# Optimization experiments

Hardware: AMD Instinct MI355X
Metric: run time of the kernel (lower is better)

Reference implementation:

```python
import jax, jax.numpy as jnp
import numpy as np

N = 100000   # nodes
E = 1600000  # edges (avg degree 16)
D = 64       # channels (in = hidden = out)
L = 3        # layers


def setup_inputs() -> dict:
    key = jax.random.key(0)
    ks = jax.random.split(key, 8)
    s = 1.0 / np.sqrt(D)
    x = jax.random.normal(ks[0], (N, D), jnp.float32)
    edge_index = jax.random.randint(ks[1], (2, E), 0, N, dtype=jnp.int32)
    edge_type = jax.random.randint(ks[2], (E,), 0, 5, dtype=jnp.int32)
    Wq = jax.random.normal(ks[3], (L, D, D), jnp.float32) * s
    Wk = jax.random.normal(ks[4], (L, D, D), jnp.float32) * s
    Wv = jax.random.normal(ks[5], (L, D, D), jnp.float32) * s
    Ws = jax.random.normal(ks[6], (L, D, D), jnp.float32) * s
    bq = jnp.zeros((L, D), jnp.float32)
    bk = jnp.zeros((L, D), jnp.float32)
    bv = jnp.zeros((L, D), jnp.float32)
    bs = jnp.zeros((L, D), jnp.float32)
    return {"x": x, "edge_index": edge_index, "edge_type": edge_type,
            "Wq": Wq, "bq": bq, "Wk": Wk, "bk": bk,
            "Wv": Wv, "bv": bv, "Ws": Ws, "bs": bs}


def _transformer_conv(x, src, dst, Wq, bq, Wk, bk, Wv, bv, Ws, bs):
    # PyG TransformerConv, heads=1, concat=True, root_weight=True, beta=False
    q = x @ Wq + bq            # [N, D]
    k = x @ Wk + bk            # [N, D]
    v = x @ Wv + bv            # [N, D]
    scale = 1.0 / jnp.sqrt(jnp.asarray(D, x.dtype))
    # per-edge attention logits: <q_i, k_j> / sqrt(D)
    alpha = jnp.sum(q[dst] * k[src], axis=-1) * scale   # [E]
    # scatter-softmax over incoming edges of each target node
    m = jax.ops.segment_max(alpha, dst, num_segments=N)  # [N]
    e = jnp.exp(alpha - m[dst])                          # [E]
    denom = jax.ops.segment_sum(e, dst, num_segments=N)  # [N]
    a = e / (denom[dst] + 1e-16)                         # [E]
    # scatter-add aggregation of alpha * v_j
    agg = jax.ops.segment_sum(a[:, None] * v[src], dst, num_segments=N)  # [N, D]
    # root/skip connection (lin_skip with bias)
    return agg + x @ Ws + bs


def reference(x, edge_index, edge_type, Wq, bq, Wk, bk, Wv, bv, Ws, bs):
    src, dst = edge_index[0], edge_index[1]
    h = x
    for i in range(L):
        h = _transformer_conv(h, src, dst, Wq[i], bq[i], Wk[i], bk[i],
                              Wv[i], bv[i], Ws[i], bs[i])
        if i < L - 1:
            h = jax.nn.relu(h)
            # F.dropout(p=0.4) is identity in eval mode
    return h
```

## Files before the change

### kernel.cpp

```cpp
#include <hip/hip_runtime.h>

#define D 64
#define LAYERS 3
#define BSHIFT 8
#define NBMAX 512
#define CHUNK 4096

typedef unsigned short ushort_t;
typedef __bf16 bf16x8 __attribute__((ext_vector_type(8)));
typedef float f32x4 __attribute__((ext_vector_type(4)));

__device__ __forceinline__ ushort_t f2bf(float f) {
    unsigned b = __float_as_uint(f);
    b += 0x7FFFu + ((b >> 16) & 1u);
    return (ushort_t)(b >> 16);
}
__device__ __forceinline__ float bflo(unsigned u) { return __uint_as_float(u << 16); }
__device__ __forceinline__ float bfhi(unsigned u) { return __uint_as_float(u & 0xFFFF0000u); }

__global__ __launch_bounds__(256) void conv_kernel(
    const float* __restrict__ x, ushort_t* __restrict__ xb, int n,
    const float* __restrict__ Wq, const float* __restrict__ Wk,
    const float* __restrict__ Wv, const float* __restrict__ Ws,
    ushort_t* __restrict__ wtb)
{
    const int t = threadIdx.x;
    if (blockIdx.x < LAYERS * 4) {
        const int b = blockIdx.x;
        const int l = b >> 2, m = b & 3;
        const float* W = ((m == 0) ? Wq : (m == 1) ? Wk : (m == 2) ? Wv : Ws)
                         + (size_t)l * D * D;
        ushort_t* out = wtb + (size_t)b * D * D;
#pragma unroll
        for (int i = 0; i < 16; ++i) {
            const int e = i * 256 + t;
            const int nn = e >> 6, k = e & 63;
            out[nn * D + k] = f2bf(W[k * D + nn]);
        }
    } else {
        const int g = (blockIdx.x - LAYERS * 4) * 256 + t;
        const int i = g * 8;
        if (i >= n) return;
        const float4 x0 = *(const float4*)(x + i);
        const float4 x1 = *(const float4*)(x + i + 4);
        uint4 u;
        u.x = (unsigned)f2bf(x0.x) | ((unsigned)f2bf(x0.y) << 16);
        u.y = (unsigned)f2bf(x0.z) | ((unsigned)f2bf(x0.w) << 16);
        u.z = (unsigned)f2bf(x1.x) | ((unsigned)f2bf(x1.y) << 16);
        u.w = (unsigned)f2bf(x1.z) | ((unsigned)f2bf(x1.w) << 16);
        *(uint4*)(xb + i) = u;
    }
}

__global__ __launch_bounds__(256) void proj_kernel(
    const ushort_t* __restrict__ hb,
    const ushort_t* __restrict__ wtb_l,
    const float* __restrict__ bq, const float* __restrict__ bk,
    const float* __restrict__ bv, const float* __restrict__ bs,
    ushort_t* __restrict__ qb, ushort_t* __restrict__ kv,
    ushort_t* __restrict__ sk, int N)
{
    __shared__ ushort_t outq[32][72];
    __shared__ ushort_t outs[32][72];
    __shared__ ushort_t outkv[32][136];

    const int t = threadIdx.x;
    const int block_row = blockIdx.x * 32;
    const int l  = t & 63;
    const int w  = t >> 6;
    const int lr = l & 15;
    const int hi = l >> 4;
    const int lk = hi * 8;

    bf16x8 afr[2][2];
#pragma unroll
    for (int rt = 0; rt < 2; ++rt) {
        const int row = block_row + rt * 16 + lr;
        const size_t base = (size_t)min(row, N - 1) * D;
#pragma unroll
        for (int ks = 0; ks < 2; ++ks)
            afr[rt][ks] = *(const bf16x8*)(hb + base + ks * 32 + lk);
    }

    const ushort_t* wtw = wtb_l + (size_t)w * D * D;
    f32x4 acc[2][4];
#pragma unroll
    for (int rt = 0; rt < 2; ++rt)
#pragma unroll
        for (int ct = 0; ct < 4; ++ct)
            acc[rt][ct] = (f32x4){0.f, 0.f, 0.f, 0.f};

#pragma unroll
    for (int ct = 0; ct < 4; ++ct) {
        const bf16x8 b0 = *(const bf16x8*)(wtw + (ct * 16 + lr) * D + lk);
        const bf16x8 b1 = *(const bf16x8*)(wtw + (ct * 16 + lr) * D + 32 + lk);
        acc[0][ct] = __builtin_amdgcn_mfma_f32_16x16x32_bf16(afr[0][0], b0, acc[0][ct], 0, 0, 0);
        acc[0][ct] = __builtin_amdgcn_mfma_f32_16x16x32_bf16(afr[0][1], b1, acc[0][ct], 0, 0, 0);
        acc[1][ct] = __builtin_amdgcn_mfma_f32_16x16x32_bf16(afr[1][0], b0, acc[1][ct], 0, 0, 0);
        acc[1][ct] = __builtin_amdgcn_mfma_f32_16x16x32_bf16(afr[1][1], b1, acc[1][ct], 0, 0, 0);
    }

    const float* biasW = (w == 0) ? bq : (w == 1) ? bk : (w == 2) ? bv : bs;
    float bcol[4];
#pragma unroll
    for (int ct = 0; ct < 4; ++ct) bcol[ct] = biasW[ct * 16 + lr];

#pragma unroll
    for (int rt = 0; rt < 2; ++rt) {
#pragma unroll
        for (int ct = 0; ct < 4; ++ct) {
#pragma unroll
            for (int r = 0; r < 4; ++r) {
                const int row = rt * 16 + hi * 4 + r;
                const int col = ct * 16 + lr;
                const ushort_t vb = f2bf(acc[rt][ct][r] + bcol[ct]);
                if (w == 0)      outq[row][col] = vb;
                else if (w == 3) outs[row][col] = vb;
                else             outkv[row][(col >> 2) * 8 + ((w == 2) ? 4 : 0) + (col & 3)] = vb;
            }
        }
    }
    __syncthreads();

    const int row  = t >> 3;
    const int ch   = (t & 7) * 8;
    const int ckv  = (t & 7) * 16;
    const int grow = block_row + row;
    if (grow < N) {
        *(uint4*)(qb + (size_t)grow * 64 + ch)       = *(const uint4*)&outq[row][ch];
        *(uint4*)(sk + (size_t)grow * 64 + ch)       = *(const uint4*)&outs[row][ch];
        *(uint4*)(kv + (size_t)grow * 128 + ckv)     = *(const uint4*)&outkv[row][ckv];
        *(uint4*)(kv + (size_t)grow * 128 + ckv + 8) = *(const uint4*)&outkv[row][ckv + 8];
    }
}

__global__ __launch_bounds__(256) void b_hist_kernel(
    const int* __restrict__ dst, int* __restrict__ bcount, int E)
{
    __shared__ int h[NBMAX];
    const int t = threadIdx.x;
    h[t] = 0; h[t + 256] = 0;
    __syncthreads();
    const int base = blockIdx.x * CHUNK;
#pragma unroll
    for (int i = 0; i < 16; ++i) {
        const int e = base + i * 256 + t;
        if (e < E) atomicAdd(h + (dst[e] >> BSHIFT), 1);
    }
    __syncthreads();
    if (h[t])       atomicAdd(bcount + t, h[t]);
    if (h[t + 256]) atomicAdd(bcount + t + 256, h[t + 256]);
}

__global__ __launch_bounds__(512) void b_scan_kernel(
    const int* __restrict__ bcount, int* __restrict__ bbase,
    int* __restrict__ gcursor, int E)
{
    __shared__ int tmp[NBMAX];
    const int t = threadIdx.x;
    const int val = bcount[t];
    tmp[t] = val;
    __syncthreads();
    for (int off = 1; off < NBMAX; off <<= 1) {
        int x = (t >= off) ? tmp[t - off] : 0;
        __syncthreads();
        tmp[t] += x;
        __syncthreads();
    }
    const int excl = tmp[t] - val;
    bbase[t] = excl;
    gcursor[t] = excl;
    if (t == NBMAX - 1) bbase[NBMAX] = E;
}

__global__ __launch_bounds__(256) void b_scatter_kernel(
    const int* __restrict__ src, const int* __restrict__ dst,
    int* __restrict__ gcursor, unsigned* __restrict__ packed, int E)
{
    __shared__ int h[NBMAX];
    __shared__ int gb[NBMAX];
    const int t = threadIdx.x;
    h[t] = 0; h[t + 256] = 0;
    __syncthreads();

    const int base = blockIdx.x * CHUNK;
    int ls[16], ld[16], lr[16];
#pragma unroll
    for (int i = 0; i < 16; ++i) {
        const int e = base + i * 256 + t;
        if (e < E) {
            ls[i] = src[e];
            ld[i] = dst[e];
            lr[i] = atomicAdd(h + (ld[i] >> BSHIFT), 1);
        }
    }
    __syncthreads();
    for (int b = t; b < NBMAX; b += 256) {
        const int c = h[b];
        gb[b] = c ? atomicAdd(gcursor + b, c) : 0;
    }
    __syncthreads();
#pragma unroll
    for (int i = 0; i < 16; ++i) {
        const int e = base + i * 256 + t;
        if (e < E) {
            const int pos = gb[ld[i] >> BSHIFT] + lr[i];
            packed[pos] = ((unsigned)(ld[i] & 255) << 24) | (unsigned)ls[i];
        }
    }
}

__global__ __launch_bounds__(256) void b_final_kernel(
    const unsigned* __restrict__ packed, const int* __restrict__ bbase,
    int* __restrict__ esrc, int* __restrict__ offs, int* __restrict__ counts,
    int N)
{
    __shared__ int hist[256];
    __shared__ int scan[256];
    __shared__ int cursor[256];
    const int t = threadIdx.x;
    const int b = blockIdx.x;
    const int s = bbase[b];
    const int e = bbase[b + 1];

    hist[t] = 0;
    __syncthreads();
    for (int j = s + t; j < e; j += 256) {
        atomicAdd(hist + (packed[j] >> 24), 1);
    }
    __syncthreads();
    const int val = hist[t];
    scan[t] = val;
    __syncthreads();
    for (int off = 1; off < 256; off <<= 1) {
        int x = (t >= off) ? scan[t - off] : 0;
        __syncthreads();
        scan[t] += x;
        __syncthreads();
    }
    const int excl = scan[t] - val;
    const int node = b * 256 + t;
    if (node < N) {
        counts[node] = val;
        offs[node]   = s + excl;
    }
    cursor[t] = excl;
    __syncthreads();
    for (int j = s + t; j < e; j += 256) {
        const unsigned p = packed[j];
        const int r = atomicAdd(cursor + (p >> 24), 1);
        esrc[s + r] = (int)(p & 0xFFFFFFu);
    }
}

__global__ __launch_bounds__(256) void node_kernel(
    const ushort_t* __restrict__ qb, const uint4* __restrict__ kv,
    const int* __restrict__ esrc, const int* __restrict__ offs,
    const int* __restrict__ counts, const ushort_t* __restrict__ sk,
    ushort_t* __restrict__ hb_out, float* __restrict__ hf_out,
    int N, int mode)
{
    const int t = threadIdx.x;
    const int lane = t & 15;
    const int node = blockIdx.x * 16 + (t >> 4);
    if (node >= N) return;

    const int start = offs[node];
    const int end   = start + counts[node];

    const uint2 qu = *(const uint2*)(qb + (size_t)node * D + lane * 4);
    float4 qv;
    qv.x = bflo(qu.x); qv.y = bfhi(qu.x);
    qv.z = bflo(qu.y); qv.w = bfhi(qu.y);

    float m = -INFINITY, ssum = 0.0f;
    float4 acc = make_float4(0.0f, 0.0f, 0.0f, 0.0f);

    int j = start;
    for (; j + 2 <= end; j += 2) {
        const int s0 = esrc[j];
        const int s1 = esrc[j + 1];
        const uint4 u0 = kv[(size_t)s0 * 16 + lane];
        const uint4 u1 = kv[(size_t)s1 * 16 + lane];

        float p0 = bflo(u0.x) * qv.x + bfhi(u0.x) * qv.y
                 + bflo(u0.y) * qv.z + bfhi(u0.y) * qv.w;
        float p1 = bflo(u1.x) * qv.x + bfhi(u1.x) * qv.y
                 + bflo(u1.y) * qv.z + bfhi(u1.y) * qv.w;
        p0 += __shfl_xor(p0, 1);  p1 += __shfl_xor(p1, 1);
        p0 += __shfl_xor(p0, 2);  p1 += __shfl_xor(p1, 2);
        p0 += __shfl_xor(p0, 4);  p1 += __shfl_xor(p1, 4);
        p0 += __shfl_xor(p0, 8);  p1 += __shfl_xor(p1, 8);
        p0 *= 0.125f;  p1 *= 0.125f;

        const float mx = fmaxf(p0, p1);
        if (mx > m) {
            const float sc = __expf(m - mx);
            ssum *= sc;
            acc.x *= sc; acc.y *= sc; acc.z *= sc; acc.w *= sc;
            m = mx;
        }
        const float w0 = __expf(p0 - m);
        const float w1 = __expf(p1 - m);
        ssum += w0 + w1;
        acc.x = fmaf(w0, bflo(u0.z), fmaf(w1, bflo(u1.z), acc.x));
        acc.y = fmaf(w0, bfhi(u0.z), fmaf(w1, bfhi(u1.z), acc.y));
        acc.z = fmaf(w0, bflo(u0.w), fmaf(w1, bflo(u1.w), acc.z));
        acc.w = fmaf(w0, bfhi(u0.w), fmaf(w1, bfhi(u1.w), acc.w));
    }
    if (j < end) {
        const int s0 = esrc[j];
        const uint4 u0 = kv[(size_t)s0 * 16 + lane];
        float p0 = bflo(u0.x) * qv.x + bfhi(u0.x) * qv.y
                 + bflo(u0.y) * qv.z + bfhi(u0.y) * qv.w;
        p0 += __shfl_xor(p0, 1);
        p0 += __shfl_xor(p0, 2);
        p0 += __shfl_xor(p0, 4);
        p0 += __shfl_xor(p0, 8);
        p0 *= 0.125f;
        if (p0 > m) {
            const float sc = __expf(m - p0);
            ssum *= sc;
            acc.x *= sc; acc.y *= sc; acc.z *= sc; acc.w *= sc;
            m = p0;
        }
        const float w0 = __expf(p0 - m);
        ssum += w0;
        acc.x = fmaf(w0, bflo(u0.z), acc.x);
        acc.y = fmaf(w0, bfhi(u0.z), acc.y);
        acc.z = fmaf(w0, bflo(u0.w), acc.z);
        acc.w = fmaf(w0, bfhi(u0.w), acc.w);
    }

    const float inv = 1.0f / (ssum + 1e-16f);
    const uint2 su = *(const uint2*)(sk + (size_t)node * D + lane * 4);
    float4 ov;
    ov.x = fmaf(acc.x, inv, bflo(su.x));
    ov.y = fmaf(acc.y, inv, bfhi(su.x));
    ov.z = fmaf(acc.z, inv, bflo(su.y));
    ov.w = fmaf(acc.w, inv, bfhi(su.y));
    if (mode == 0) {
        ov.x = fmaxf(ov.x, 0.0f); ov.y = fmaxf(ov.y, 0.0f);
        ov.z = fmaxf(ov.z, 0.0f); ov.w = fmaxf(ov.w, 0.0f);
        uint2 u;
        u.x = (unsigned)f2bf(ov.x) | ((unsigned)f2bf(ov.y) << 16);
        u.y = (unsigned)f2bf(ov.z) | ((unsigned)f2bf(ov.w) << 16);
        *(uint2*)(hb_out + (size_t)node * D + lane * 4) = u;
    } else {
        *(float4*)(hf_out + (size_t)node * D + lane * 4) = ov;
    }
}

extern "C" void kernel_launch(void* const* d_in, const int* in_sizes, int n_in,
                              void* d_out, int out_size, void* d_ws, size_t ws_size,
                              hipStream_t stream)
{
    const float* x   = (const float*)d_in[0];
    const int* ei    = (const int*)d_in[1];
    const float* Wq  = (const float*)d_in[3];
    const float* bq  = (const float*)d_in[4];
    const float* Wk  = (const float*)d_in[5];
    const float* bk  = (const float*)d_in[6];
    const float* Wv  = (const float*)d_in[7];
    const float* bv  = (const float*)d_in[8];
    const float* Ws  = (const float*)d_in[9];
    const float* bs  = (const float*)d_in[10];

    const int N = in_sizes[0] / D;
    const int E = in_sizes[2];
    const int* src = ei;
    const int* dst = ei + E;
    const int NB = (N + 255) / 256;

    ushort_t* xb  = (ushort_t*)d_ws;
    ushort_t* hb0 = xb  + (size_t)N * D;
    ushort_t* hb1 = hb0 + (size_t)N * D;
    ushort_t* qb  = hb1 + (size_t)N * D;
    ushort_t* sk  = qb  + (size_t)N * D;
    ushort_t* kv  = sk  + (size_t)N * D;
    ushort_t* wtb = kv  + (size_t)N * 128;
    int* esrc     = (int*)(wtb + LAYERS * 4 * D * D);
    unsigned* packed = (unsigned*)(esrc + E);
    int* counts  = (int*)(packed + E);
    int* offs    = counts + NBMAX * 256;
    int* bcount  = offs + NBMAX * 256;
    int* bbase   = bcount + NBMAX;
    int* gcursor = bbase + NBMAX + 1;

    const int conv_x_blocks = (N * D + 2047) / 2048;
    conv_kernel<<<LAYERS * 4 + conv_x_blocks, 256, 0, stream>>>(
        x, xb, N * D, Wq, Wk, Wv, Ws, wtb);

    hipMemsetAsync(bcount, 0, NBMAX * 4, stream);
    const int p1_blocks = (E + CHUNK - 1) / CHUNK;
    b_hist_kernel<<<p1_blocks, 256, 0, stream>>>(dst, bcount, E);
    b_scan_kernel<<<1, NBMAX, 0, stream>>>(bcount, bbase, gcursor, E);
    b_scatter_kernel<<<p1_blocks, 256, 0, stream>>>(src, dst, gcursor, packed, E);
    b_final_kernel<<<NB, 256, 0, stream>>>(packed, bbase, esrc, offs, counts, N);

    const int proj_blocks = (N + 31) / 32;
    const int node_blocks = (N + 15) / 16;

    const ushort_t* cur = xb;
    for (int l = 0; l < LAYERS; ++l) {
        const int last = (l == LAYERS - 1);
        ushort_t* hb_out = (l & 1) ? hb1 : hb0;

        proj_kernel<<<proj_blocks, 256, 0, stream>>>(
            cur, wtb + (size_t)l * 4 * D * D,
            bq + (size_t)l * D, bk + (size_t)l * D,
            bv + (size_t)l * D, bs + (size_t)l * D,
            qb, kv, sk, N);

        node_kernel<<<node_blocks, 256, 0, stream>>>(
            qb, (const uint4*)kv, esrc, offs, counts, sk,
            hb_out, (float*)d_out, N, last ? 1 : 0);

        cur = hb_out;
    }
}
```

Baseline: 343.8 us.

## Fuse next-layer projection into aggregation kernel and drop online softmax max

The per-node aggregation kernel now also runs the next layer's Q/K/V/skip projection. It stages each block's 16 ReLU'd bf16 hidden rows in shared memory and feeds them to MFMA, so the hidden state no longer makes a round trip through global memory and separate projection launches disappear. The x-to-bf16 conversion moves into the first projection kernel, and the bcount memset moves into the weight-conversion kernel. The online softmax max tracking is removed and exp is applied to the raw scaled logits, which saves rescaling work but risks overflow if logits grow large.

Result: no change. 348.1 us (+1.2%).

```diff
diff --git a/kernel.cpp b/kernel.cpp
--- a/kernel.cpp
+++ b/kernel.cpp
@@ -19,10 +19,9 @@
 __device__ __forceinline__ float bfhi(unsigned u) { return __uint_as_float(u & 0xFFFF0000u); }
 
 __global__ __launch_bounds__(256) void conv_kernel(
-    const float* __restrict__ x, ushort_t* __restrict__ xb, int n,
     const float* __restrict__ Wq, const float* __restrict__ Wk,
     const float* __restrict__ Wv, const float* __restrict__ Ws,
-    ushort_t* __restrict__ wtb)
+    ushort_t* __restrict__ wtb, int* __restrict__ bcount)
 {
     const int t = threadIdx.x;
     if (blockIdx.x < LAYERS * 4) {
@@ -38,22 +37,13 @@
             out[nn * D + k] = f2bf(W[k * D + nn]);
         }
     } else {
-        const int g = (blockIdx.x - LAYERS * 4) * 256 + t;
-        const int i = g * 8;
-        if (i >= n) return;
-        const float4 x0 = *(const float4*)(x + i);
-        const float4 x1 = *(const float4*)(x + i + 4);
-        uint4 u;
-        u.x = (unsigned)f2bf(x0.x) | ((unsigned)f2bf(x0.y) << 16);
-        u.y = (unsigned)f2bf(x0.z) | ((unsigned)f2bf(x0.w) << 16);
-        u.z = (unsigned)f2bf(x1.x) | ((unsigned)f2bf(x1.y) << 16);
-        u.w = (unsigned)f2bf(x1.z) | ((unsigned)f2bf(x1.w) << 16);
-        *(uint4*)(xb + i) = u;
-    }
-}
-
-__global__ __launch_bounds__(256) void proj_kernel(
-    const ushort_t* __restrict__ hb,
+        bcount[t] = 0;
+        bcount[t + 256] = 0;
+    }
+}
+
+__global__ __launch_bounds__(256) void proj0_kernel(
+    const float* __restrict__ x,
     const ushort_t* __restrict__ wtb_l,
     const float* __restrict__ bq, const float* __restrict__ bk,
     const float* __restrict__ bv, const float* __restrict__ bs,
@@ -76,10 +66,15 @@
 #pragma unroll
     for (int rt = 0; rt < 2; ++rt) {
         const int row = block_row + rt * 16 + lr;
-        const size_t base = (size_t)min(row, N - 1) * D;
-#pragma unroll
-        for (int ks = 0; ks < 2; ++ks)
-            afr[rt][ks] = *(const bf16x8*)(hb + base + ks * 32 + lk);
+        const float* xr = x + (size_t)min(row, N - 1) * D;
+#pragma unroll
+        for (int ks = 0; ks < 2; ++ks) {
+            const float4 a = *(const float4*)(xr + ks * 32 + lk);
+            const float4 b = *(const float4*)(xr + ks * 32 + lk + 4);
+            ushort_t* rp = (ushort_t*)&afr[rt][ks];
+            rp[0] = f2bf(a.x); rp[1] = f2bf(a.y); rp[2] = f2bf(a.z); rp[3] = f2bf(a.w);
+            rp[4] = f2bf(b.x); rp[5] = f2bf(b.y); rp[6] = f2bf(b.z); rp[7] = f2bf(b.w);
+        }
     }
 
     const ushort_t* wtw = wtb_l + (size_t)w * D * D;
@@ -253,35 +248,44 @@
     }
 }
 
-__global__ __launch_bounds__(256) void node_kernel(
-    const ushort_t* __restrict__ qb, const uint4* __restrict__ kv,
+__global__ __launch_bounds__(256) void nodeAB_kernel(
+    const ushort_t* __restrict__ qb_in, const uint4* __restrict__ kv_in,
     const int* __restrict__ esrc, const int* __restrict__ offs,
-    const int* __restrict__ counts, const ushort_t* __restrict__ sk,
-    ushort_t* __restrict__ hb_out, float* __restrict__ hf_out,
-    int N, int mode)
-{
+    const int* __restrict__ counts, const ushort_t* __restrict__ sk_in,
+    const ushort_t* __restrict__ wtb_next,
+    const float* __restrict__ bq, const float* __restrict__ bk,
+    const float* __restrict__ bv, const float* __restrict__ bs,
+    ushort_t* __restrict__ qb_out, ushort_t* __restrict__ kv_out,
+    ushort_t* __restrict__ sk_out, int N)
+{
+    __shared__ ushort_t hs[16][72];
+    __shared__ ushort_t outq[16][72];
+    __shared__ ushort_t outs[16][72];
+    __shared__ ushort_t outkv[16][136];
+
     const int t = threadIdx.x;
     const int lane = t & 15;
-    const int node = blockIdx.x * 16 + (t >> 4);
-    if (node >= N) return;
-
-    const int start = offs[node];
-    const int end   = start + counts[node];
-
-    const uint2 qu = *(const uint2*)(qb + (size_t)node * D + lane * 4);
+    const int g = t >> 4;
+    const int node = blockIdx.x * 16 + g;
+    const int nodec = min(node, N - 1);
+
+    const int start = offs[nodec];
+    const int end   = start + counts[nodec];
+
+    const uint2 qu = *(const uint2*)(qb_in + (size_t)nodec * D + lane * 4);
     float4 qv;
     qv.x = bflo(qu.x); qv.y = bfhi(qu.x);
     qv.z = bflo(qu.y); qv.w = bfhi(qu.y);
 
-    float m = -INFINITY, ssum = 0.0f;
+    float ssum = 0.0f;
     float4 acc = make_float4(0.0f, 0.0f, 0.0f, 0.0f);
 
     int j = start;
     for (; j + 2 <= end; j += 2) {
         const int s0 = esrc[j];
         const int s1 = esrc[j + 1];
-        const uint4 u0 = kv[(size_t)s0 * 16 + lane];
-        const uint4 u1 = kv[(size_t)s1 * 16 + lane];
+        const uint4 u0 = kv_in[(size_t)s0 * 16 + lane];
+        const uint4 u1 = kv_in[(size_t)s1 * 16 + lane];
 
         float p0 = bflo(u0.x) * qv.x + bfhi(u0.x) * qv.y
                  + bflo(u0.y) * qv.z + bfhi(u0.y) * qv.w;
@@ -291,17 +295,146 @@
         p0 += __shfl_xor(p0, 2);  p1 += __shfl_xor(p1, 2);
         p0 += __shfl_xor(p0, 4);  p1 += __shfl_xor(p1, 4);
         p0 += __shfl_xor(p0, 8);  p1 += __shfl_xor(p1, 8);
-        p0 *= 0.125f;  p1 *= 0.125f;
-
-        const float mx = fmaxf(p0, p1);
-        if (mx > m) {
-            const float sc = __expf(m - mx);
-            ssum *= sc;
-            acc.x *= sc; acc.y *= sc; acc.z *= sc; acc.w *= sc;
-            m = mx;
-        }
-        const float w0 = __expf(p0 - m);
-        const float w1 = __expf(p1 - m);
+
+        const float w0 = __expf(p0 * 0.125f);
+        const float w1 = __expf(p1 * 0.125f);
+        ssum += w0 + w1;
+        acc.x = fmaf(w0, bflo(u0.z), fmaf(w1, bflo(u1.z), acc.x));
+        acc.y = fmaf(w0, bfhi(u0.z), fmaf(w1, bfhi(u1.z), acc.y));
+        acc.z = fmaf(w0, bflo(u0.w), fmaf(w1, bflo(u1.w), acc.z));
+        acc.w = fmaf(w0, bfhi(u0.w), fmaf(w1, bfhi(u1.w), acc.w));
+    }
+    if (j < end) {
+        const int s0 = esrc[j];
+        const uint4 u0 = kv_in[(size_t)s0 * 16 + lane];
+        float p0 = bflo(u0.x) * qv.x + bfhi(u0.x) * qv.y
+                 + bflo(u0.y) * qv.z + bfhi(u0.y) * qv.w;
+        p0 += __shfl_xor(p0, 1);
+        p0 += __shfl_xor(p0, 2);
+        p0 += __shfl_xor(p0, 4);
+        p0 += __shfl_xor(p0, 8);
+        const float w0 = __expf(p0 * 0.125f);
+        ssum += w0;
+        acc.x = fmaf(w0, bflo(u0.z), acc.x);
+        acc.y = fmaf(w0, bfhi(u0.z), acc.y);
+        acc.z = fmaf(w0, bflo(u0.w), acc.z);
+        acc.w = fmaf(w0, bfhi(u0.w), acc.w);
+    }
+
+    const float inv = 1.0f / (ssum + 1e-16f);
+    const uint2 su = *(const uint2*)(sk_in + (size_t)nodec * D + lane * 4);
+    float4 ov;
+    ov.x = fmaxf(fmaf(acc.x, inv, bflo(su.x)), 0.0f);
+    ov.y = fmaxf(fmaf(acc.y, inv, bfhi(su.x)), 0.0f);
+    ov.z = fmaxf(fmaf(acc.z, inv, bflo(su.y)), 0.0f);
+    ov.w = fmaxf(fmaf(acc.w, inv, bfhi(su.y)), 0.0f);
+
+    uint2 hv;
+    hv.x = (unsigned)f2bf(ov.x) | ((unsigned)f2bf(ov.y) << 16);
+    hv.y = (unsigned)f2bf(ov.z) | ((unsigned)f2bf(ov.w) << 16);
+    *(uint2*)&hs[g][lane * 4] = hv;
+    __syncthreads();
+
+    const int l  = t & 63;
+    const int w  = t >> 6;
+    const int lr = l & 15;
+    const int hi = l >> 4;
+    const int lk = hi * 8;
+
+    bf16x8 afr[2];
+#pragma unroll
+    for (int ks = 0; ks < 2; ++ks)
+        afr[ks] = *(const bf16x8*)&hs[lr][ks * 32 + lk];
+
+    const ushort_t* wtw = wtb_next + (size_t)w * D * D;
+    f32x4 accp[4];
+#pragma unroll
+    for (int ct = 0; ct < 4; ++ct) accp[ct] = (f32x4){0.f, 0.f, 0.f, 0.f};
+
+#pragma unroll
+    for (int ct = 0; ct < 4; ++ct) {
+        const bf16x8 b0 = *(const bf16x8*)(wtw + (ct * 16 + lr) * D + lk);
+        const bf16x8 b1 = *(const bf16x8*)(wtw + (ct * 16 + lr) * D + 32 + lk);
+        accp[ct] = __builtin_amdgcn_mfma_f32_16x16x32_bf16(afr[0], b0, accp[ct], 0, 0, 0);
+        accp[ct] = __builtin_amdgcn_mfma_f32_16x16x32_bf16(afr[1], b1, accp[ct], 0, 0, 0);
+    }
+
+    const float* biasW = (w == 0) ? bq : (w == 1) ? bk : (w == 2) ? bv : bs;
+#pragma unroll
+    for (int ct = 0; ct < 4; ++ct) {
+        const float bcol = biasW[ct * 16 + lr];
+#pragma unroll
+        for (int r = 0; r < 4; ++r) {
+            const int row = hi * 4 + r;
+            const int col = ct * 16 + lr;
+            const ushort_t vb = f2bf(accp[ct][r] + bcol);
+            if (w == 0)      outq[row][col] = vb;
+            else if (w == 3) outs[row][col] = vb;
+            else             outkv[row][(col >> 2) * 8 + ((w == 2) ? 4 : 0) + (col & 3)] = vb;
+        }
+    }
+    __syncthreads();
+
+    {
+        const int row = t >> 4;
+        const int ck  = (t & 15) * 8;
+        const int grow = blockIdx.x * 16 + row;
+        if (grow < N)
+            *(uint4*)(kv_out + (size_t)grow * 128 + ck) = *(const uint4*)&outkv[row][ck];
+    }
+    {
+        const int row = (t & 127) >> 3;
+        const int ch  = (t & 7) * 8;
+        const int grow = blockIdx.x * 16 + row;
+        if (grow < N) {
+            if (t < 128)
+                *(uint4*)(qb_out + (size_t)grow * 64 + ch) = *(const uint4*)&outq[row][ch];
+            else
+                *(uint4*)(sk_out + (size_t)grow * 64 + ch) = *(const uint4*)&outs[row][ch];
+        }
+    }
+}
+
+__global__ __launch_bounds__(256) void nodeC_kernel(
+    const ushort_t* __restrict__ qb, const uint4* __restrict__ kv,
+    const int* __restrict__ esrc, const int* __restrict__ offs,
+    const int* __restrict__ counts, const ushort_t* __restrict__ sk,
+    float* __restrict__ hout, int N)
+{
+    const int t = threadIdx.x;
+    const int lane = t & 15;
+    const int node = blockIdx.x * 16 + (t >> 4);
+    if (node >= N) return;
+
+    const int start = offs[node];
+    const int end   = start + counts[node];
+
+    const uint2 qu = *(const uint2*)(qb + (size_t)node * D + lane * 4);
+    float4 qv;
+    qv.x = bflo(qu.x); qv.y = bfhi(qu.x);
+    qv.z = bflo(qu.y); qv.w = bfhi(qu.y);
+
+    float ssum = 0.0f;
+    float4 acc = make_float4(0.0f, 0.0f, 0.0f, 0.0f);
+
+    int j = start;
+    for (; j + 2 <= end; j += 2) {
+        const int s0 = esrc[j];
+        const int s1 = esrc[j + 1];
+        const uint4 u0 = kv[(size_t)s0 * 16 + lane];
+        const uint4 u1 = kv[(size_t)s1 * 16 + lane];
+
+        float p0 = bflo(u0.x) * qv.x + bfhi(u0.x) * qv.y
+                 + bflo(u0.y) * qv.z + bfhi(u0.y) * qv.w;
+        float p1 = bflo(u1.x) * qv.x + bfhi(u1.x) * qv.y
+                 + bflo(u1.y) * qv.z + bfhi(u1.y) * qv.w;
+        p0 += __shfl_xor(p0, 1);  p1 += __shfl_xor(p1, 1);
+        p0 += __shfl_xor(p0, 2);  p1 += __shfl_xor(p1, 2);
+        p0 += __shfl_xor(p0, 4);  p1 += __shfl_xor(p1, 4);
+        p0 += __shfl_xor(p0, 8);  p1 += __shfl_xor(p1, 8);
+
+        const float w0 = __expf(p0 * 0.125f);
+        const float w1 = __expf(p1 * 0.125f);
         ssum += w0 + w1;
         acc.x = fmaf(w0, bflo(u0.z), fmaf(w1, bflo(u1.z), acc.x));
         acc.y = fmaf(w0, bfhi(u0.z), fmaf(w1, bfhi(u1.z), acc.y));
@@ -317,14 +450,7 @@
         p0 += __shfl_xor(p0, 2);
         p0 += __shfl_xor(p0, 4);
         p0 += __shfl_xor(p0, 8);
-        p0 *= 0.125f;
-        if (p0 > m) {
-            const float sc = __expf(m - p0);
-            ssum *= sc;
-            acc.x *= sc; acc.y *= sc; acc.z *= sc; acc.w *= sc;
-            m = p0;
-        }
-        const float w0 = __expf(p0 - m);
+        const float w0 = __expf(p0 * 0.125f);
         ssum += w0;
         acc.x = fmaf(w0, bflo(u0.z), acc.x);
         acc.y = fmaf(w0, bfhi(u0.z), acc.y);
@@ -339,16 +465,7 @@
     ov.y = fmaf(acc.y, inv, bfhi(su.x));
     ov.z = fmaf(acc.z, inv, bflo(su.y));
     ov.w = fmaf(acc.w, inv, bfhi(su.y));
-    if (mode == 0) {
-        ov.x = fmaxf(ov.x, 0.0f); ov.y = fmaxf(ov.y, 0.0f);
-        ov.z = fmaxf(ov.z, 0.0f); ov.w = fmaxf(ov.w, 0.0f);
-        uint2 u;
-        u.x = (unsigned)f2bf(ov.x) | ((unsigned)f2bf(ov.y) << 16);
-        u.y = (unsigned)f2bf(ov.z) | ((unsigned)f2bf(ov.w) << 16);
-        *(uint2*)(hb_out + (size_t)node * D + lane * 4) = u;
-    } else {
-        *(float4*)(hf_out + (size_t)node * D + lane * 4) = ov;
-    }
+    *(float4*)(hout + (size_t)node * D + lane * 4) = ov;
 }
 
 extern "C" void kernel_launch(void* const* d_in, const int* in_sizes, int n_in,
@@ -372,13 +489,13 @@
     const int* dst = ei + E;
     const int NB = (N + 255) / 256;
 
-    ushort_t* xb  = (ushort_t*)d_ws;
-    ushort_t* hb0 = xb  + (size_t)N * D;
-    ushort_t* hb1 = hb0 + (size_t)N * D;
-    ushort_t* qb  = hb1 + (size_t)N * D;
-    ushort_t* sk  = qb  + (size_t)N * D;
-    ushort_t* kv  = sk  + (size_t)N * D;
-    ushort_t* wtb = kv  + (size_t)N * 128;
+    ushort_t* q0  = (ushort_t*)d_ws;
+    ushort_t* sk0 = q0  + (size_t)N * D;
+    ushort_t* kv0 = sk0 + (size_t)N * D;
+    ushort_t* q1  = kv0 + (size_t)N * 128;
+    ushort_t* sk1 = q1  + (size_t)N * D;
+    ushort_t* kv1 = sk1 + (size_t)N * D;
+    ushort_t* wtb = kv1 + (size_t)N * 128;
     int* esrc     = (int*)(wtb + LAYERS * 4 * D * D);
     unsigned* packed = (unsigned*)(esrc + E);
     int* counts  = (int*)(packed + E);
@@ -387,11 +504,8 @@
     int* bbase   = bcount + NBMAX;
     int* gcursor = bbase + NBMAX + 1;
 
-    const int conv_x_blocks = (N * D + 2047) / 2048;
-    conv_kernel<<<LAYERS * 4 + conv_x_blocks, 256, 0, stream>>>(
-        x, xb, N * D, Wq, Wk, Wv, Ws, wtb);
-
-    hipMemsetAsync(bcount, 0, NBMAX * 4, stream);
+    conv_kernel<<<LAYERS * 4 + 1, 256, 0, stream>>>(Wq, Wk, Wv, Ws, wtb, bcount);
+
     const int p1_blocks = (E + CHUNK - 1) / CHUNK;
     b_hist_kernel<<<p1_blocks, 256, 0, stream>>>(dst, bcount, E);
     b_scan_kernel<<<1, NBMAX, 0, stream>>>(bcount, bbase, gcursor, E);
@@ -401,21 +515,22 @@
     const int proj_blocks = (N + 31) / 32;
     const int node_blocks = (N + 15) / 16;
 
-    const ushort_t* cur = xb;
-    for (int l = 0; l < LAYERS; ++l) {
-        const int last = (l == LAYERS - 1);
-        ushort_t* hb_out = (l & 1) ? hb1 : hb0;
-
-        proj_kernel<<<proj_blocks, 256, 0, stream>>>(
-            cur, wtb + (size_t)l * 4 * D * D,
-            bq + (size_t)l * D, bk + (size_t)l * D,
-            bv + (size_t)l * D, bs + (size_t)l * D,
-            qb, kv, sk, N);
-
-        node_kernel<<<node_blocks, 256, 0, stream>>>(
-            qb, (const uint4*)kv, esrc, offs, counts, sk,
-            hb_out, (float*)d_out, N, last ? 1 : 0);
-
-        cur = hb_out;
-    }
-}
+    proj0_kernel<<<proj_blocks, 256, 0, stream>>>(
+        x, wtb, bq, bk, bv, bs, q0, kv0, sk0, N);
+
+    nodeAB_kernel<<<node_blocks, 256, 0, stream>>>(
+        q0, (const uint4*)kv0, esrc, offs, counts, sk0,
+        wtb + (size_t)1 * 4 * D * D,
+        bq + D, bk + D, bv + D, bs + D,
+        q1, kv1, sk1, N);
+
+    nodeAB_kernel<<<node_blocks, 256, 0, stream>>>(
+        q1, (const uint4*)kv1, esrc, offs, counts, sk1,
+        wtb + (size_t)2 * 4 * D * D,
+        bq + 2 * D, bk + 2 * D, bv + 2 * D, bs + 2 * D,
+        q0, kv0, sk0, N);
+
+    nodeC_kernel<<<node_blocks, 256, 0, stream>>>(
+        q0, (const uint4*)kv0, esrc, offs, counts, sk0,
+        (float*)d_out, N);
+}
```
